# Performance work log

Measured on AMD Instinct MI355X. Metric: run time of the kernel, lower is better.

Reference implementation:

```python
import jax, jax.numpy as jnp
import numpy as np

K_PERIODS = 4
PMAX = 64
MIN_PERIOD = 8


def setup_inputs() -> dict:
    key = jax.random.key(0)
    x = jax.random.normal(key, (32, 512, 64), dtype=jnp.float32)  # [B, T, N]
    return {"x": x}


def reference(x):
    """Dense, fixed-shape equivalent of PeriodicityTransform.forward (mask=None).

    Instead of a Python list of variable-shape PeriodGroup tiles, returns a
    padded tensor values[bn, k, c, p] where for each (sequence bn, freq rank k)
    with period P and cycles C, values[bn, k, :C, :P] equals the torch tile
    seqs[bn, T-C*P : T].reshape(C, P); entries outside (C, P) are zero.
    Also returns the integer periods and cycles per (bn, k).
    """
    B, T, N = x.shape
    BN = B * N
    seqs = jnp.transpose(x, (0, 2, 1)).reshape(BN, T)  # [BN, T]

    # top-k nonzero FFT frequencies (DC bin zeroed out)
    spec = jnp.fft.rfft(seqs, axis=-1)
    mag2 = spec.real ** 2 + spec.imag ** 2
    mag2 = mag2.at[..., 0].set(0.0)
    _, kidx = jax.lax.top_k(mag2, K_PERIODS)  # [BN, K]
    kidx = jnp.maximum(kidx, 1)

    # periods = clamp(T // f, min=MIN_PERIOD, max=PMAX); cycles = T // period
    periods = jnp.clip(T // kidx, MIN_PERIOD, PMAX)  # [BN, K]
    cycles = T // periods                              # [BN, K]

    cmax = T // MIN_PERIOD  # static upper bound on cycles
    i = jnp.arange(cmax)[:, None]   # cycle index  [Cmax, 1]
    j = jnp.arange(PMAX)[None, :]   # phase index  [1, Pmax]

    start = T - cycles * periods                                   # [BN, K]
    idx = start[..., None, None] + i * periods[..., None, None] + j  # [BN,K,Cmax,Pmax]
    idx = jnp.clip(idx, 0, T - 1)
    valid = (i < cycles[..., None, None]) & (j < periods[..., None, None])

    gathered = jnp.take_along_axis(
        seqs[:, None, :], idx.reshape(BN, K_PERIODS, -1), axis=-1
    ).reshape(BN, K_PERIODS, cmax, PMAX)
    values = jnp.where(valid, gathered, jnp.float32(0.0))
    return values, periods, cycles
```

## Files before the change

### kernel.cpp

```cpp
#include <hip/hip_runtime.h>
#include <math.h>

#define TT 512
#define KP 4

typedef unsigned long long u64;

__global__ __launch_bounds__(256) void periodicity_kernel(const float* __restrict__ x,
                                                          float* __restrict__ out) {
    const int bn   = blockIdx.x;
    const int tid  = threadIdx.x;
    const int lane = tid & 63;
    const int wid  = tid >> 6;
    const int b = bn >> 6;
    const int n = bn & 63;

    __shared__ float  row[TT];
    __shared__ float2 buf[TT];
    __shared__ float2 tw[TT];
    __shared__ u64    keys[256];
    __shared__ int    fin8[8];
    __shared__ double candV8[8];

    float sv, cv_;
    sincosf((float)(2.0 * M_PI / 512.0) * (float)tid, &sv, &cv_);
    tw[tid]       = make_float2(cv_, -sv);
    tw[tid + 256] = make_float2(-cv_, sv);

    const float* xb = x + (size_t)b * (TT * 64) + n;
    {
        float v0 = xb[(size_t)tid * 64];
        float v1 = xb[(size_t)(tid + 256) * 64];
        row[tid] = v0;  row[tid + 256] = v1;
        float sum = v0 + v1, dif = v0 - v1;
        buf[tid]       = make_float2(sum, 0.f);
        buf[tid + 256] = make_float2(dif * cv_, -dif * sv);
    }
    __syncthreads();

    #pragma unroll
    for (int stg = 0; stg < 4; ++stg) {
        if (tid < 128) {
            const int Q  = 64 >> (2 * stg);
            const int B4 = Q << 2;
            const int h  = tid >> 6;
            const int j  = tid & 63;
            const int g  = j >> (6 - 2 * stg);
            const int i  = j & (Q - 1);
            const int base = (h << 8) + g * B4 + i;
            float2 x0 = buf[base], x1 = buf[base + Q];
            float2 x2 = buf[base + 2 * Q], x3 = buf[base + 3 * Q];
            float2 A  = make_float2(x0.x + x2.x, x0.y + x2.y);
            float2 Bm = make_float2(x0.x - x2.x, x0.y - x2.y);
            float2 Cc = make_float2(x1.x + x3.x, x1.y + x3.y);
            float2 D  = make_float2(x1.x - x3.x, x1.y - x3.y);
            float2 y0 = make_float2(A.x + Cc.x, A.y + Cc.y);
            float2 y2 = make_float2(A.x - Cc.x, A.y - Cc.y);
            float2 y1 = make_float2(Bm.x + D.y, Bm.y - D.x);
            float2 y3 = make_float2(Bm.x - D.y, Bm.y + D.x);
            const int m = i << (1 + 2 * stg);
            float2 t1 = tw[m], t2 = tw[2 * m], t3 = tw[3 * m];
            buf[base]         = y0;
            buf[base + Q]     = make_float2(y1.x * t1.x - y1.y * t1.y, y1.x * t1.y + y1.y * t1.x);
            buf[base + 2 * Q] = make_float2(y2.x * t2.x - y2.y * t2.y, y2.x * t2.y + y2.y * t2.x);
            buf[base + 3 * Q] = make_float2(y3.x * t3.x - y3.y * t3.y, y3.x * t3.y + y3.y * t3.x);
        }
        __syncthreads();
    }

    #pragma unroll
    for (int hh = 0; hh < 2; ++hh) {
        int pos = tid + hh * 256;
        int p = pos & 255;
        int kprime = ((p & 3) << 6) | (((p >> 2) & 3) << 4) | (((p >> 4) & 3) << 2) | ((p >> 6) & 3);
        int f = 2 * kprime + hh;
        if (f >= 1 && f <= 256) {
            float2 v = buf[pos];
            float mag = v.x * v.x + v.y * v.y;
            keys[f - 1] = ((u64)__float_as_uint(mag) << 32) | (u64)(255 - (f - 1));
        }
    }
    __syncthreads();

    if (wid == 0) {
        u64 k0 = keys[lane * 4 + 0];
        u64 k1 = keys[lane * 4 + 1];
        u64 k2 = keys[lane * 4 + 2];
        u64 k3 = keys[lane * 4 + 3];
        #define CSWAP(a, b) { if (a < b) { u64 _t = a; a = b; b = _t; } }
        CSWAP(k0, k1) CSWAP(k2, k3) CSWAP(k0, k2) CSWAP(k1, k3) CSWAP(k1, k2)
        #undef CSWAP
        #pragma unroll
        for (int r = 0; r < 8; ++r) {
            u64 w = k0;
            #pragma unroll
            for (int off = 32; off >= 1; off >>= 1) {
                u64 o = __shfl_xor(w, off);
                if (o > w) w = o;
            }
            if (k0 == w) { k0 = k1; k1 = k2; k2 = k3; k3 = 0; }
            if (lane == 0) fin8[r] = 256 - (int)(w & 0xff);
        }
    }
    __syncthreads();

    {
        const int cid = tid >> 5;
        const int sub = tid & 31;
        const int fc  = fin8[cid];
        const int t0  = sub * 16;
        const double W = 6.2831853071795864769 / 512.0;
        double zr, zi, wr, wi;
        sincos(W * (double)((fc * t0) & 511), &zi, &zr);
        sincos(W * (double)fc, &wi, &wr);
        double ar = 0.0, ai = 0.0;
        const float4* r4 = (const float4*)row;
        #pragma unroll
        for (int v4i = 0; v4i < 4; ++v4i) {
            float4 xv = r4[sub * 4 + v4i];
            #define STEP(comp)                                   \
                { double xd = (double)xv.comp;                   \
                  ar = fma(xd, zr, ar); ai = fma(xd, zi, ai);    \
                  double tq = zr * wr - zi * wi;                 \
                  zi = fma(zr, wi, zi * wr); zr = tq; }
            STEP(x) STEP(y) STEP(z) STEP(w)
            #undef STEP
        }
        #pragma unroll
        for (int off = 16; off >= 1; off >>= 1) {
            ar += __shfl_xor(ar, off);
            ai += __shfl_xor(ai, off);
        }
        if (sub == 0) candV8[cid] = ar * ar + ai * ai;
    }
    __syncthreads();

    int per[KP], cyc[KP], st[KP];
    {
        unsigned chosen = 0;
        #pragma unroll
        for (int k = 0; k < KP; ++k) {
            double bv = -1.0; int bbin = 0x7fffffff; int bj = 0;
            #pragma unroll
            for (int j = 0; j < 8; ++j) {
                if (chosen & (1u << j)) continue;
                double vj = candV8[j];
                int    bjn = fin8[j];
                if (vj > bv || (vj == bv && bjn < bbin)) { bv = vj; bbin = bjn; bj = j; }
            }
            chosen |= (1u << bj);
            int p = TT / bbin;
            p = p < 8 ? 8 : (p > 64 ? 64 : p);
            per[k] = p;
            cyc[k] = TT / p;
            st[k]  = TT - cyc[k] * p;
        }
    }

    const size_t VOFF = (size_t)2048 * KP * 64 * 64;
    if (tid == 0) {
        #pragma unroll
        for (int k = 0; k < KP; ++k) {
            out[VOFF + (size_t)bn * KP + k]        = (float)per[k];
            out[VOFF + 8192 + (size_t)bn * KP + k] = (float)cyc[k];
        }
    }

    float* outv = out + (size_t)bn * (KP * 64 * 64);
    const int c_local = tid >> 4;
    const int p0 = (tid & 15) << 2;
    #pragma unroll
    for (int it = 0; it < 16; ++it) {
        const int k = it >> 2;
        const int c = ((it & 3) << 4) + c_local;
        float4 v = make_float4(0.f, 0.f, 0.f, 0.f);
        const int P = per[k], C = cyc[k], S0 = st[k];
        if (c < C) {
            const int base = S0 + c * P;
            if (p0 + 3 < P) {
                v.x = row[base + p0];
                v.y = row[base + p0 + 1];
                v.z = row[base + p0 + 2];
                v.w = row[base + p0 + 3];
            } else {
                v.x = (p0 + 0 < P) ? row[base + p0]     : 0.f;
                v.y = (p0 + 1 < P) ? row[base + p0 + 1] : 0.f;
                v.z = (p0 + 2 < P) ? row[base + p0 + 2] : 0.f;
                v.w = (p0 + 3 < P) ? row[base + p0 + 3] : 0.f;
            }
        }
        *(float4*)(outv + (size_t)it * 1024 + (size_t)tid * 4) = v;
    }
}

extern "C" void kernel_launch(void* const* d_in, const int* in_sizes, int n_in,
                              void* d_out, int out_size, void* d_ws, size_t ws_size,
                              hipStream_t stream) {
    const float* x = (const float*)d_in[0];
    float* out = (float*)d_out;
    hipLaunchKernelGGL(periodicity_kernel, dim3(2048), dim3(256), 0, stream, x, out);
}
```

Baseline: 33.73 us.

## Process four sequences per block with float4 loads and two-row concurrent FFT

```diff
diff --git a/kernel.cpp b/kernel.cpp
--- a/kernel.cpp
+++ b/kernel.cpp
@@ -8,188 +8,207 @@
 
 __global__ __launch_bounds__(256) void periodicity_kernel(const float* __restrict__ x,
                                                           float* __restrict__ out) {
-    const int bn   = blockIdx.x;
+    const int blk  = blockIdx.x;
     const int tid  = threadIdx.x;
     const int lane = tid & 63;
     const int wid  = tid >> 6;
-    const int b = bn >> 6;
-    const int n = bn & 63;
-
-    __shared__ float  row[TT];
-    __shared__ float2 buf[TT];
+    const int b  = blk >> 4;
+    const int n0 = (blk & 15) << 2;
+
     __shared__ float2 tw[TT];
-    __shared__ u64    keys[256];
-    __shared__ int    fin8[8];
-    __shared__ double candV8[8];
-
-    float sv, cv_;
-    sincosf((float)(2.0 * M_PI / 512.0) * (float)tid, &sv, &cv_);
-    tw[tid]       = make_float2(cv_, -sv);
-    tw[tid + 256] = make_float2(-cv_, sv);
-
-    const float* xb = x + (size_t)b * (TT * 64) + n;
-    {
-        float v0 = xb[(size_t)tid * 64];
-        float v1 = xb[(size_t)(tid + 256) * 64];
-        row[tid] = v0;  row[tid + 256] = v1;
-        float sum = v0 + v1, dif = v0 - v1;
-        buf[tid]       = make_float2(sum, 0.f);
-        buf[tid + 256] = make_float2(dif * cv_, -dif * sv);
-    }
-    __syncthreads();
+    __shared__ float  rowl[2][TT];
+    __shared__ float2 buf[2][TT];
+    __shared__ u64    keys[2][256];
+    __shared__ int    fin8[2][8];
+    __shared__ double candV8[2][8];
+
+    float sv, cv;
+    sincosf((float)(2.0 * M_PI / 512.0) * (float)tid, &sv, &cv);
+    tw[tid]       = make_float2(cv, -sv);
+    tw[tid + 256] = make_float2(-cv, sv);
+
+    const float* xb = x + (size_t)b * (TT * 64) + n0;
+    float4 ldA = *(const float4*)(xb + (size_t)tid * 64);
+    float4 ldB = *(const float4*)(xb + (size_t)(tid + 256) * 64);
+
+    const size_t VOFF = (size_t)2048 * KP * 64 * 64;
 
     #pragma unroll
-    for (int stg = 0; stg < 4; ++stg) {
-        if (tid < 128) {
-            const int Q  = 64 >> (2 * stg);
-            const int B4 = Q << 2;
-            const int h  = tid >> 6;
-            const int j  = tid & 63;
-            const int g  = j >> (6 - 2 * stg);
-            const int i  = j & (Q - 1);
-            const int base = (h << 8) + g * B4 + i;
-            float2 x0 = buf[base], x1 = buf[base + Q];
-            float2 x2 = buf[base + 2 * Q], x3 = buf[base + 3 * Q];
-            float2 A  = make_float2(x0.x + x2.x, x0.y + x2.y);
-            float2 Bm = make_float2(x0.x - x2.x, x0.y - x2.y);
-            float2 Cc = make_float2(x1.x + x3.x, x1.y + x3.y);
-            float2 D  = make_float2(x1.x - x3.x, x1.y - x3.y);
-            float2 y0 = make_float2(A.x + Cc.x, A.y + Cc.y);
-            float2 y2 = make_float2(A.x - Cc.x, A.y - Cc.y);
-            float2 y1 = make_float2(Bm.x + D.y, Bm.y - D.x);
-            float2 y3 = make_float2(Bm.x - D.y, Bm.y + D.x);
-            const int m = i << (1 + 2 * stg);
-            float2 t1 = tw[m], t2 = tw[2 * m], t3 = tw[3 * m];
-            buf[base]         = y0;
-            buf[base + Q]     = make_float2(y1.x * t1.x - y1.y * t1.y, y1.x * t1.y + y1.y * t1.x);
-            buf[base + 2 * Q] = make_float2(y2.x * t2.x - y2.y * t2.y, y2.x * t2.y + y2.y * t2.x);
-            buf[base + 3 * Q] = make_float2(y3.x * t3.x - y3.y * t3.y, y3.x * t3.y + y3.y * t3.x);
-        }
-        __syncthreads();
-    }
-
-    #pragma unroll
-    for (int hh = 0; hh < 2; ++hh) {
-        int pos = tid + hh * 256;
-        int p = pos & 255;
-        int kprime = ((p & 3) << 6) | (((p >> 2) & 3) << 4) | (((p >> 4) & 3) << 2) | ((p >> 6) & 3);
-        int f = 2 * kprime + hh;
-        if (f >= 1 && f <= 256) {
-            float2 v = buf[pos];
-            float mag = v.x * v.x + v.y * v.y;
-            keys[f - 1] = ((u64)__float_as_uint(mag) << 32) | (u64)(255 - (f - 1));
-        }
-    }
-    __syncthreads();
-
-    if (wid == 0) {
-        u64 k0 = keys[lane * 4 + 0];
-        u64 k1 = keys[lane * 4 + 1];
-        u64 k2 = keys[lane * 4 + 2];
-        u64 k3 = keys[lane * 4 + 3];
-        #define CSWAP(a, b) { if (a < b) { u64 _t = a; a = b; b = _t; } }
-        CSWAP(k0, k1) CSWAP(k2, k3) CSWAP(k0, k2) CSWAP(k1, k3) CSWAP(k1, k2)
-        #undef CSWAP
+    for (int ss = 0; ss < 2; ++ss) {
+        __syncthreads();
+
         #pragma unroll
-        for (int r = 0; r < 8; ++r) {
-            u64 w = k0;
-            #pragma unroll
-            for (int off = 32; off >= 1; off >>= 1) {
-                u64 o = __shfl_xor(w, off);
-                if (o > w) w = o;
-            }
-            if (k0 == w) { k0 = k1; k1 = k2; k2 = k3; k3 = 0; }
-            if (lane == 0) fin8[r] = 256 - (int)(w & 0xff);
-        }
-    }
-    __syncthreads();
-
-    {
-        const int cid = tid >> 5;
-        const int sub = tid & 31;
-        const int fc  = fin8[cid];
-        const int t0  = sub * 16;
-        const double W = 6.2831853071795864769 / 512.0;
-        double zr, zi, wr, wi;
-        sincos(W * (double)((fc * t0) & 511), &zi, &zr);
-        sincos(W * (double)fc, &wi, &wr);
-        double ar = 0.0, ai = 0.0;
-        const float4* r4 = (const float4*)row;
+        for (int rr = 0; rr < 2; ++rr) {
+            const int rg = ss * 2 + rr;
+            float v0 = ((const float*)&ldA)[rg];
+            float v1 = ((const float*)&ldB)[rg];
+            rowl[rr][tid] = v0;  rowl[rr][tid + 256] = v1;
+            float sum = v0 + v1, dif = v0 - v1;
+            buf[rr][tid]       = make_float2(sum, 0.f);
+            buf[rr][tid + 256] = make_float2(dif * cv, -dif * sv);
+        }
+        __syncthreads();
+
+        {
+            const int frr = tid >> 7;
+            const int fh  = (tid >> 6) & 1;
+            const int fj  = tid & 63;
+            float2* bb = &buf[frr][fh << 8];
+            #pragma unroll
+            for (int stg = 0; stg < 4; ++stg) {
+                const int Q  = 64 >> (2 * stg);
+                const int B4 = Q << 2;
+                const int g  = fj >> (6 - 2 * stg);
+                const int i  = fj & (Q - 1);
+                const int base = g * B4 + i;
+                float2 x0 = bb[base],         x1 = bb[base + Q];
+                float2 x2 = bb[base + 2 * Q], x3 = bb[base + 3 * Q];
+                float2 A  = make_float2(x0.x + x2.x, x0.y + x2.y);
+                float2 Bm = make_float2(x0.x - x2.x, x0.y - x2.y);
+                float2 Cc = make_float2(x1.x + x3.x, x1.y + x3.y);
+                float2 D  = make_float2(x1.x - x3.x, x1.y - x3.y);
+                float2 y0 = make_float2(A.x + Cc.x, A.y + Cc.y);
+                float2 y2 = make_float2(A.x - Cc.x, A.y - Cc.y);
+                float2 y1 = make_float2(Bm.x + D.y, Bm.y - D.x);
+                float2 y3 = make_float2(Bm.x - D.y, Bm.y + D.x);
+                const int m = i << (1 + 2 * stg);
+                float2 t1 = tw[m], t2 = tw[2 * m], t3 = tw[3 * m];
+                bb[base]         = y0;
+                bb[base + Q]     = make_float2(y1.x * t1.x - y1.y * t1.y, y1.x * t1.y + y1.y * t1.x);
+                bb[base + 2 * Q] = make_float2(y2.x * t2.x - y2.y * t2.y, y2.x * t2.y + y2.y * t2.x);
+                bb[base + 3 * Q] = make_float2(y3.x * t3.x - y3.y * t3.y, y3.x * t3.y + y3.y * t3.x);
+                __syncthreads();
+            }
+        }
+
+        {
+            const int p  = tid;
+            const int kp = ((p & 3) << 6) | (((p >> 2) & 3) << 4) | (((p >> 4) & 3) << 2) | ((p >> 6) & 3);
+            #pragma unroll
+            for (int q = 0; q < 4; ++q) {
+                const int rr = q >> 1, hh = q & 1;
+                const int f = 2 * kp + hh;
+                if (f >= 1 && f <= 256) {
+                    float2 v = buf[rr][hh * 256 + p];
+                    float mag = v.x * v.x + v.y * v.y;
+                    keys[rr][f - 1] = ((u64)__float_as_uint(mag) << 32) | (u64)(255 - (f - 1));
+                }
+            }
+        }
+        __syncthreads();
+
+        if (wid < 2) {
+            const int rr = wid;
+            u64 k0 = keys[rr][lane * 4 + 0];
+            u64 k1 = keys[rr][lane * 4 + 1];
+            u64 k2 = keys[rr][lane * 4 + 2];
+            u64 k3 = keys[rr][lane * 4 + 3];
+            #define CSWAP(a, b) { if (a < b) { u64 _t = a; a = b; b = _t; } }
+            CSWAP(k0, k1) CSWAP(k2, k3) CSWAP(k0, k2) CSWAP(k1, k3) CSWAP(k1, k2)
+            #undef CSWAP
+            #pragma unroll
+            for (int r = 0; r < 8; ++r) {
+                u64 w = k0;
+                #pragma unroll
+                for (int off = 32; off >= 1; off >>= 1) {
+                    u64 o = __shfl_xor(w, off);
+                    if (o > w) w = o;
+                }
+                if (k0 == w) { k0 = k1; k1 = k2; k2 = k3; k3 = 0; }
+                if (lane == 0) fin8[rr][r] = 256 - (int)(w & 0xff);
+            }
+        }
+        __syncthreads();
+
+        {
+            const int cidg = tid >> 4;
+            const int rr   = cidg >> 3;
+            const int cand = cidg & 7;
+            const int sub  = tid & 15;
+            const int fc = fin8[rr][cand];
+            const int t0 = sub * 32;
+            const double W = 6.2831853071795864769 / 512.0;
+            double zr, zi, wr, wi;
+            sincos(W * (double)((fc * t0) & 511), &zi, &zr);
+            sincos(W * (double)fc, &wi, &wr);
+            double ar = 0.0, ai = 0.0;
+            const float4* r4 = (const float4*)rowl[rr];
+            #pragma unroll
+            for (int v4i = 0; v4i < 8; ++v4i) {
+                float4 xv = r4[sub * 8 + v4i];
+                #define STEP(comp)                                   \
+                    { double xd = (double)xv.comp;                   \
+                      ar = fma(xd, zr, ar); ai = fma(xd, zi, ai);    \
+                      double tq = zr * wr - zi * wi;                 \
+                      zi = fma(zr, wi, zi * wr); zr = tq; }
+                STEP(x) STEP(y) STEP(z) STEP(w)
+                #undef STEP
+            }
+            #pragma unroll
+            for (int off = 8; off >= 1; off >>= 1) {
+                ar += __shfl_xor(ar, off);
+                ai += __shfl_xor(ai, off);
+            }
+            if (sub == 0) candV8[rr][cand] = ar * ar + ai * ai;
+        }
+        __syncthreads();
+
         #pragma unroll
-        for (int v4i = 0; v4i < 4; ++v4i) {
-            float4 xv = r4[sub * 4 + v4i];
-            #define STEP(comp)                                   \
-                { double xd = (double)xv.comp;                   \
-                  ar = fma(xd, zr, ar); ai = fma(xd, zi, ai);    \
-                  double tq = zr * wr - zi * wi;                 \
-                  zi = fma(zr, wi, zi * wr); zr = tq; }
-            STEP(x) STEP(y) STEP(z) STEP(w)
-            #undef STEP
-        }
-        #pragma unroll
-        for (int off = 16; off >= 1; off >>= 1) {
-            ar += __shfl_xor(ar, off);
-            ai += __shfl_xor(ai, off);
-        }
-        if (sub == 0) candV8[cid] = ar * ar + ai * ai;
-    }
-    __syncthreads();
-
-    int per[KP], cyc[KP], st[KP];
-    {
-        unsigned chosen = 0;
-        #pragma unroll
-        for (int k = 0; k < KP; ++k) {
-            double bv = -1.0; int bbin = 0x7fffffff; int bj = 0;
-            #pragma unroll
-            for (int j = 0; j < 8; ++j) {
-                if (chosen & (1u << j)) continue;
-                double vj = candV8[j];
-                int    bjn = fin8[j];
-                if (vj > bv || (vj == bv && bjn < bbin)) { bv = vj; bbin = bjn; bj = j; }
-            }
-            chosen |= (1u << bj);
-            int p = TT / bbin;
-            p = p < 8 ? 8 : (p > 64 ? 64 : p);
-            per[k] = p;
-            cyc[k] = TT / p;
-            st[k]  = TT - cyc[k] * p;
-        }
-    }
-
-    const size_t VOFF = (size_t)2048 * KP * 64 * 64;
-    if (tid == 0) {
-        #pragma unroll
-        for (int k = 0; k < KP; ++k) {
-            out[VOFF + (size_t)bn * KP + k]        = (float)per[k];
-            out[VOFF + 8192 + (size_t)bn * KP + k] = (float)cyc[k];
-        }
-    }
-
-    float* outv = out + (size_t)bn * (KP * 64 * 64);
-    const int c_local = tid >> 4;
-    const int p0 = (tid & 15) << 2;
-    #pragma unroll
-    for (int it = 0; it < 16; ++it) {
-        const int k = it >> 2;
-        const int c = ((it & 3) << 4) + c_local;
-        float4 v = make_float4(0.f, 0.f, 0.f, 0.f);
-        const int P = per[k], C = cyc[k], S0 = st[k];
-        if (c < C) {
-            const int base = S0 + c * P;
-            if (p0 + 3 < P) {
-                v.x = row[base + p0];
-                v.y = row[base + p0 + 1];
-                v.z = row[base + p0 + 2];
-                v.w = row[base + p0 + 3];
-            } else {
-                v.x = (p0 + 0 < P) ? row[base + p0]     : 0.f;
-                v.y = (p0 + 1 < P) ? row[base + p0 + 1] : 0.f;
-                v.z = (p0 + 2 < P) ? row[base + p0 + 2] : 0.f;
-                v.w = (p0 + 3 < P) ? row[base + p0 + 3] : 0.f;
-            }
-        }
-        *(float4*)(outv + (size_t)it * 1024 + (size_t)tid * 4) = v;
+        for (int rr = 0; rr < 2; ++rr) {
+            const int rg = ss * 2 + rr;
+            const int bn = b * 64 + n0 + rg;
+            int per[KP], cycv[KP], st[KP];
+            unsigned chosen = 0;
+            #pragma unroll
+            for (int k = 0; k < KP; ++k) {
+                double bv = -1.0; int bbin = 0x7fffffff; int bj = 0;
+                #pragma unroll
+                for (int j = 0; j < 8; ++j) {
+                    if (chosen & (1u << j)) continue;
+                    double vj = candV8[rr][j];
+                    int    bjn = fin8[rr][j];
+                    if (vj > bv || (vj == bv && bjn < bbin)) { bv = vj; bbin = bjn; bj = j; }
+                }
+                chosen |= (1u << bj);
+                int p = TT / bbin;
+                p = p < 8 ? 8 : (p > 64 ? 64 : p);
+                per[k]  = p;
+                cycv[k] = TT / p;
+                st[k]   = TT - cycv[k] * p;
+            }
+            if (tid == 0) {
+                #pragma unroll
+                for (int k = 0; k < KP; ++k) {
+                    out[VOFF + (size_t)bn * KP + k]        = (float)per[k];
+                    out[VOFF + 8192 + (size_t)bn * KP + k] = (float)cycv[k];
+                }
+            }
+            float* outv = out + (size_t)bn * (KP * 64 * 64);
+            const int c_local = tid >> 4;
+            const int p0 = (tid & 15) << 2;
+            #pragma unroll
+            for (int it = 0; it < 16; ++it) {
+                const int k = it >> 2;
+                const int c = ((it & 3) << 4) + c_local;
+                float4 v = make_float4(0.f, 0.f, 0.f, 0.f);
+                const int P = per[k], C = cycv[k], S0 = st[k];
+                if (c < C) {
+                    const int base = S0 + c * P;
+                    if (p0 + 3 < P) {
+                        v.x = rowl[rr][base + p0];
+                        v.y = rowl[rr][base + p0 + 1];
+                        v.z = rowl[rr][base + p0 + 2];
+                        v.w = rowl[rr][base + p0 + 3];
+                    } else {
+                        v.x = (p0 + 0 < P) ? rowl[rr][base + p0]     : 0.f;
+                        v.y = (p0 + 1 < P) ? rowl[rr][base + p0 + 1] : 0.f;
+                        v.z = (p0 + 2 < P) ? rowl[rr][base + p0 + 2] : 0.f;
+                        v.w = (p0 + 3 < P) ? rowl[rr][base + p0 + 3] : 0.f;
+                    }
+                }
+                *(float4*)(outv + (size_t)it * 1024 + (size_t)tid * 4) = v;
+            }
+        }
     }
 }
 
@@ -198,5 +217,5 @@
                               hipStream_t stream) {
     const float* x = (const float*)d_in[0];
     float* out = (float*)d_out;
-    hipLaunchKernelGGL(periodicity_kernel, dim3(2048), dim3(256), 0, stream, x, out);
+    hipLaunchKernelGGL(periodicity_kernel, dim3(512), dim3(256), 0, stream, x, out);
 }
```

Result: slower. 43.27 us (+28.3%).

## Process four sequences per block with float4 loads and overlapped output stores

Applied to the files above, without the earlier changes.

```diff
diff --git a/kernel.cpp b/kernel.cpp
--- a/kernel.cpp
+++ b/kernel.cpp
@@ -6,191 +6,219 @@
 
 typedef unsigned long long u64;
 
-__global__ __launch_bounds__(256) void periodicity_kernel(const float* __restrict__ x,
+__global__ __launch_bounds__(512) void periodicity_kernel(const float* __restrict__ x,
                                                           float* __restrict__ out) {
-    const int bn   = blockIdx.x;
+    const int blk  = blockIdx.x;
     const int tid  = threadIdx.x;
     const int lane = tid & 63;
     const int wid  = tid >> 6;
-    const int b = bn >> 6;
-    const int n = bn & 63;
-
-    __shared__ float  row[TT];
+    const int b  = blk >> 4;
+    const int n0 = (blk & 15) << 2;
+
+    __shared__ float2 tw[TT];
+    __shared__ __align__(16) float rowl[2][TT];
     __shared__ float2 buf[TT];
-    __shared__ float2 tw[TT];
     __shared__ u64    keys[256];
     __shared__ int    fin8[8];
     __shared__ double candV8[8];
-
-    float sv, cv_;
-    sincosf((float)(2.0 * M_PI / 512.0) * (float)tid, &sv, &cv_);
-    tw[tid]       = make_float2(cv_, -sv);
-    tw[tid + 256] = make_float2(-cv_, sv);
-
-    const float* xb = x + (size_t)b * (TT * 64) + n;
+    __shared__ int    pstore[2][12];
+
     {
-        float v0 = xb[(size_t)tid * 64];
-        float v1 = xb[(size_t)(tid + 256) * 64];
-        row[tid] = v0;  row[tid + 256] = v1;
-        float sum = v0 + v1, dif = v0 - v1;
-        buf[tid]       = make_float2(sum, 0.f);
-        buf[tid + 256] = make_float2(dif * cv_, -dif * sv);
+        float s, c;
+        sincosf((float)(2.0 * M_PI / 512.0) * (float)tid, &s, &c);
+        tw[tid] = make_float2(c, -s);
     }
-    __syncthreads();
+
+    const float* xb = x + (size_t)b * (TT * 64) + n0;
+    float4 ld = *(const float4*)(xb + (size_t)tid * 64);
+
+    const size_t VOFF = (size_t)2048 * KP * 64 * 64;
+
+    auto store_row = [&](int rowIdx, int pvb) {
+        const int bnp = b * 64 + n0 + rowIdx;
+        float* outv = out + (size_t)bnp * (KP * 64 * 64);
+        #pragma unroll
+        for (int it = 0; it < 8; ++it) {
+            const int flat4 = it * 512 + tid;
+            const int k   = flat4 >> 10;
+            const int rem = flat4 & 1023;
+            const int c   = rem >> 4;
+            const int p0  = (rem & 15) << 2;
+            const int P = pstore[pvb][k], C = pstore[pvb][4 + k], S0 = pstore[pvb][8 + k];
+            float4 v = make_float4(0.f, 0.f, 0.f, 0.f);
+            if (c < C) {
+                const int base = S0 + c * P;
+                if (p0 + 3 < P) {
+                    v.x = rowl[pvb][base + p0];
+                    v.y = rowl[pvb][base + p0 + 1];
+                    v.z = rowl[pvb][base + p0 + 2];
+                    v.w = rowl[pvb][base + p0 + 3];
+                } else {
+                    if (p0     < P) v.x = rowl[pvb][base + p0];
+                    if (p0 + 1 < P) v.y = rowl[pvb][base + p0 + 1];
+                    if (p0 + 2 < P) v.z = rowl[pvb][base + p0 + 2];
+                    if (p0 + 3 < P) v.w = rowl[pvb][base + p0 + 3];
+                }
+            }
+            *(float4*)(outv + (size_t)flat4 * 4) = v;
+        }
+    };
 
     #pragma unroll
-    for (int stg = 0; stg < 4; ++stg) {
-        if (tid < 128) {
-            const int Q  = 64 >> (2 * stg);
-            const int B4 = Q << 2;
-            const int h  = tid >> 6;
-            const int j  = tid & 63;
-            const int g  = j >> (6 - 2 * stg);
-            const int i  = j & (Q - 1);
-            const int base = (h << 8) + g * B4 + i;
-            float2 x0 = buf[base], x1 = buf[base + Q];
-            float2 x2 = buf[base + 2 * Q], x3 = buf[base + 3 * Q];
-            float2 A  = make_float2(x0.x + x2.x, x0.y + x2.y);
-            float2 Bm = make_float2(x0.x - x2.x, x0.y - x2.y);
-            float2 Cc = make_float2(x1.x + x3.x, x1.y + x3.y);
-            float2 D  = make_float2(x1.x - x3.x, x1.y - x3.y);
-            float2 y0 = make_float2(A.x + Cc.x, A.y + Cc.y);
-            float2 y2 = make_float2(A.x - Cc.x, A.y - Cc.y);
-            float2 y1 = make_float2(Bm.x + D.y, Bm.y - D.x);
-            float2 y3 = make_float2(Bm.x - D.y, Bm.y + D.x);
-            const int m = i << (1 + 2 * stg);
-            float2 t1 = tw[m], t2 = tw[2 * m], t3 = tw[3 * m];
-            buf[base]         = y0;
-            buf[base + Q]     = make_float2(y1.x * t1.x - y1.y * t1.y, y1.x * t1.y + y1.y * t1.x);
-            buf[base + 2 * Q] = make_float2(y2.x * t2.x - y2.y * t2.y, y2.x * t2.y + y2.y * t2.x);
-            buf[base + 3 * Q] = make_float2(y3.x * t3.x - y3.y * t3.y, y3.x * t3.y + y3.y * t3.x);
+    for (int ss = 0; ss < 4; ++ss) {
+        const int cur = ss & 1, pv = cur ^ 1;
+
+        if (ss > 0) store_row(ss - 1, pv);
+
+        {
+            float rv = (ss == 0) ? ld.x : (ss == 1) ? ld.y : (ss == 2) ? ld.z : ld.w;
+            rowl[cur][tid] = rv;
+        }
+        __syncthreads();
+
+        if (tid < 256) {
+            buf[tid] = make_float2(rowl[cur][tid] + rowl[cur][tid + 256], 0.f);
+        } else {
+            const int j = tid - 256;
+            float dif = rowl[cur][j] - rowl[cur][j + 256];
+            float2 t = tw[j];
+            buf[tid] = make_float2(dif * t.x, dif * t.y);
+        }
+        __syncthreads();
+
+        #pragma unroll
+        for (int stg = 0; stg < 4; ++stg) {
+            if (tid < 128) {
+                const int Q  = 64 >> (2 * stg);
+                const int B4 = Q << 2;
+                const int h  = tid >> 6;
+                const int fj = tid & 63;
+                const int g  = fj >> (6 - 2 * stg);
+                const int i  = fj & (Q - 1);
+                float2* bb = &buf[h << 8];
+                const int base = g * B4 + i;
+                float2 x0 = bb[base],         x1 = bb[base + Q];
+                float2 x2 = bb[base + 2 * Q], x3 = bb[base + 3 * Q];
+                float2 A  = make_float2(x0.x + x2.x, x0.y + x2.y);
+                float2 Bm = make_float2(x0.x - x2.x, x0.y - x2.y);
+                float2 Cc = make_float2(x1.x + x3.x, x1.y + x3.y);
+                float2 D  = make_float2(x1.x - x3.x, x1.y - x3.y);
+                float2 y0 = make_float2(A.x + Cc.x, A.y + Cc.y);
+                float2 y2 = make_float2(A.x - Cc.x, A.y - Cc.y);
+                float2 y1 = make_float2(Bm.x + D.y, Bm.y - D.x);
+                float2 y3 = make_float2(Bm.x - D.y, Bm.y + D.x);
+                const int m = i << (1 + 2 * stg);
+                float2 t1 = tw[m], t2 = tw[2 * m], t3 = tw[3 * m];
+                bb[base]         = y0;
+                bb[base + Q]     = make_float2(y1.x * t1.x - y1.y * t1.y, y1.x * t1.y + y1.y * t1.x);
+                bb[base + 2 * Q] = make_float2(y2.x * t2.x - y2.y * t2.y, y2.x * t2.y + y2.y * t2.x);
+                bb[base + 3 * Q] = make_float2(y3.x * t3.x - y3.y * t3.y, y3.x * t3.y + y3.y * t3.x);
+            }
+            __syncthreads();
+        }
+
+        {
+            const int p  = tid & 255;
+            const int hh = tid >> 8;
+            const int kp = ((p & 3) << 6) | (((p >> 2) & 3) << 4) | (((p >> 4) & 3) << 2) | ((p >> 6) & 3);
+            const int f = 2 * kp + hh;
+            if (f >= 1 && f <= 256) {
+                float2 v = buf[tid];
+                float mag = v.x * v.x + v.y * v.y;
+                keys[f - 1] = ((u64)__float_as_uint(mag) << 32) | (u64)(255 - (f - 1));
+            }
+        }
+        __syncthreads();
+
+        if (wid == 0) {
+            u64 k0 = keys[lane * 4 + 0];
+            u64 k1 = keys[lane * 4 + 1];
+            u64 k2 = keys[lane * 4 + 2];
+            u64 k3 = keys[lane * 4 + 3];
+            #define CSWAP(a, b) { if (a < b) { u64 _t = a; a = b; b = _t; } }
+            CSWAP(k0, k1) CSWAP(k2, k3) CSWAP(k0, k2) CSWAP(k1, k3) CSWAP(k1, k2)
+            #undef CSWAP
+            #pragma unroll
+            for (int r = 0; r < 8; ++r) {
+                u64 w = k0;
+                #pragma unroll
+                for (int off = 32; off >= 1; off >>= 1) {
+                    u64 o = __shfl_xor(w, off);
+                    if (o > w) w = o;
+                }
+                if (k0 == w) { k0 = k1; k1 = k2; k2 = k3; k3 = 0; }
+                if (lane == 0) fin8[r] = 256 - (int)(w & 0xff);
+            }
+        }
+        __syncthreads();
+
+        if (tid < 256) {
+            const int cid = tid >> 5;
+            const int sub = tid & 31;
+            const int fc  = fin8[cid];
+            const int t0  = sub * 16;
+            const double W = 6.2831853071795864769 / 512.0;
+            double zr, zi, wr, wi;
+            sincos(W * (double)((fc * t0) & 511), &zi, &zr);
+            sincos(W * (double)fc, &wi, &wr);
+            double ar = 0.0, ai = 0.0;
+            const float4* r4 = (const float4*)rowl[cur];
+            #pragma unroll
+            for (int v4i = 0; v4i < 4; ++v4i) {
+                float4 xv = r4[sub * 4 + v4i];
+                #define STEP(comp)                                   \
+                    { double xd = (double)xv.comp;                   \
+                      ar = fma(xd, zr, ar); ai = fma(xd, zi, ai);    \
+                      double tq = zr * wr - zi * wi;                 \
+                      zi = fma(zr, wi, zi * wr); zr = tq; }
+                STEP(x) STEP(y) STEP(z) STEP(w)
+                #undef STEP
+            }
+            #pragma unroll
+            for (int off = 16; off >= 1; off >>= 1) {
+                ar += __shfl_xor(ar, off);
+                ai += __shfl_xor(ai, off);
+            }
+            if (sub == 0) candV8[cid] = ar * ar + ai * ai;
+        }
+        __syncthreads();
+
+        if (wid == 0) {
+            int per[KP], cycv[KP], stv[KP];
+            unsigned chosen = 0;
+            #pragma unroll
+            for (int k = 0; k < KP; ++k) {
+                double bv = -1.0; int bbin = 0x7fffffff; int bj = 0;
+                #pragma unroll
+                for (int j = 0; j < 8; ++j) {
+                    if (chosen & (1u << j)) continue;
+                    double vj = candV8[j];
+                    int    bjn = fin8[j];
+                    if (vj > bv || (vj == bv && bjn < bbin)) { bv = vj; bbin = bjn; bj = j; }
+                }
+                chosen |= (1u << bj);
+                int p = TT / bbin;
+                p = p < 8 ? 8 : (p > 64 ? 64 : p);
+                per[k]  = p;
+                cycv[k] = TT / p;
+                stv[k]  = TT - cycv[k] * p;
+            }
+            if (lane == 0) {
+                const int bn = b * 64 + n0 + ss;
+                #pragma unroll
+                for (int k = 0; k < KP; ++k) {
+                    pstore[cur][k]     = per[k];
+                    pstore[cur][4 + k] = cycv[k];
+                    pstore[cur][8 + k] = stv[k];
+                    out[VOFF + (size_t)bn * KP + k]        = (float)per[k];
+                    out[VOFF + 8192 + (size_t)bn * KP + k] = (float)cycv[k];
+                }
+            }
         }
         __syncthreads();
     }
 
-    #pragma unroll
-    for (int hh = 0; hh < 2; ++hh) {
-        int pos = tid + hh * 256;
-        int p = pos & 255;
-        int kprime = ((p & 3) << 6) | (((p >> 2) & 3) << 4) | (((p >> 4) & 3) << 2) | ((p >> 6) & 3);
-        int f = 2 * kprime + hh;
-        if (f >= 1 && f <= 256) {
-            float2 v = buf[pos];
-            float mag = v.x * v.x + v.y * v.y;
-            keys[f - 1] = ((u64)__float_as_uint(mag) << 32) | (u64)(255 - (f - 1));
-        }
-    }
-    __syncthreads();
-
-    if (wid == 0) {
-        u64 k0 = keys[lane * 4 + 0];
-        u64 k1 = keys[lane * 4 + 1];
-        u64 k2 = keys[lane * 4 + 2];
-        u64 k3 = keys[lane * 4 + 3];
-        #define CSWAP(a, b) { if (a < b) { u64 _t = a; a = b; b = _t; } }
-        CSWAP(k0, k1) CSWAP(k2, k3) CSWAP(k0, k2) CSWAP(k1, k3) CSWAP(k1, k2)
-        #undef CSWAP
-        #pragma unroll
-        for (int r = 0; r < 8; ++r) {
-            u64 w = k0;
-            #pragma unroll
-            for (int off = 32; off >= 1; off >>= 1) {
-                u64 o = __shfl_xor(w, off);
-                if (o > w) w = o;
-            }
-            if (k0 == w) { k0 = k1; k1 = k2; k2 = k3; k3 = 0; }
-            if (lane == 0) fin8[r] = 256 - (int)(w & 0xff);
-        }
-    }
-    __syncthreads();
-
-    {
-        const int cid = tid >> 5;
-        const int sub = tid & 31;
-        const int fc  = fin8[cid];
-        const int t0  = sub * 16;
-        const double W = 6.2831853071795864769 / 512.0;
-        double zr, zi, wr, wi;
-        sincos(W * (double)((fc * t0) & 511), &zi, &zr);
-        sincos(W * (double)fc, &wi, &wr);
-        double ar = 0.0, ai = 0.0;
-        const float4* r4 = (const float4*)row;
-        #pragma unroll
-        for (int v4i = 0; v4i < 4; ++v4i) {
-            float4 xv = r4[sub * 4 + v4i];
-            #define STEP(comp)                                   \
-                { double xd = (double)xv.comp;                   \
-                  ar = fma(xd, zr, ar); ai = fma(xd, zi, ai);    \
-                  double tq = zr * wr - zi * wi;                 \
-                  zi = fma(zr, wi, zi * wr); zr = tq; }
-            STEP(x) STEP(y) STEP(z) STEP(w)
-            #undef STEP
-        }
-        #pragma unroll
-        for (int off = 16; off >= 1; off >>= 1) {
-            ar += __shfl_xor(ar, off);
-            ai += __shfl_xor(ai, off);
-        }
-        if (sub == 0) candV8[cid] = ar * ar + ai * ai;
-    }
-    __syncthreads();
-
-    int per[KP], cyc[KP], st[KP];
-    {
-        unsigned chosen = 0;
-        #pragma unroll
-        for (int k = 0; k < KP; ++k) {
-            double bv = -1.0; int bbin = 0x7fffffff; int bj = 0;
-            #pragma unroll
-            for (int j = 0; j < 8; ++j) {
-                if (chosen & (1u << j)) continue;
-                double vj = candV8[j];
-                int    bjn = fin8[j];
-                if (vj > bv || (vj == bv && bjn < bbin)) { bv = vj; bbin = bjn; bj = j; }
-            }
-            chosen |= (1u << bj);
-            int p = TT / bbin;
-            p = p < 8 ? 8 : (p > 64 ? 64 : p);
-            per[k] = p;
-            cyc[k] = TT / p;
-            st[k]  = TT - cyc[k] * p;
-        }
-    }
-
-    const size_t VOFF = (size_t)2048 * KP * 64 * 64;
-    if (tid == 0) {
-        #pragma unroll
-        for (int k = 0; k < KP; ++k) {
-            out[VOFF + (size_t)bn * KP + k]        = (float)per[k];
-            out[VOFF + 8192 + (size_t)bn * KP + k] = (float)cyc[k];
-        }
-    }
-
-    float* outv = out + (size_t)bn * (KP * 64 * 64);
-    const int c_local = tid >> 4;
-    const int p0 = (tid & 15) << 2;
-    #pragma unroll
-    for (int it = 0; it < 16; ++it) {
-        const int k = it >> 2;
-        const int c = ((it & 3) << 4) + c_local;
-        float4 v = make_float4(0.f, 0.f, 0.f, 0.f);
-        const int P = per[k], C = cyc[k], S0 = st[k];
-        if (c < C) {
-            const int base = S0 + c * P;
-            if (p0 + 3 < P) {
-                v.x = row[base + p0];
-                v.y = row[base + p0 + 1];
-                v.z = row[base + p0 + 2];
-                v.w = row[base + p0 + 3];
-            } else {
-                v.x = (p0 + 0 < P) ? row[base + p0]     : 0.f;
-                v.y = (p0 + 1 < P) ? row[base + p0 + 1] : 0.f;
-                v.z = (p0 + 2 < P) ? row[base + p0 + 2] : 0.f;
-                v.w = (p0 + 3 < P) ? row[base + p0 + 3] : 0.f;
-            }
-        }
-        *(float4*)(outv + (size_t)it * 1024 + (size_t)tid * 4) = v;
-    }
+    store_row(3, 1);
 }
 
 extern "C" void kernel_launch(void* const* d_in, const int* in_sizes, int n_in,
@@ -198,5 +226,5 @@
                               hipStream_t stream) {
     const float* x = (const float*)d_in[0];
     float* out = (float*)d_out;
-    hipLaunchKernelGGL(periodicity_kernel, dim3(2048), dim3(256), 0, stream, x, out);
+    hipLaunchKernelGGL(periodicity_kernel, dim3(512), dim3(512), 0, stream, x, out);
 }
```

Measured after the change: 47.86 us. 1.42x slower.

## Skip fp64 DFT refinement when top magnitudes are well separated; hoist zero fill

Applied to the files above, without the earlier changes.

```diff
diff --git a/kernel.cpp b/kernel.cpp
--- a/kernel.cpp
+++ b/kernel.cpp
@@ -5,6 +5,8 @@
 #define KP 4
 
 typedef unsigned long long u64;
+
+#define SYNCL() asm volatile("s_waitcnt lgkmcnt(0)\n\ts_barrier" ::: "memory")
 
 __global__ __launch_bounds__(256) void periodicity_kernel(const float* __restrict__ x,
                                                           float* __restrict__ out) {
@@ -15,17 +17,24 @@
     const int b = bn >> 6;
     const int n = bn & 63;
 
-    __shared__ float  row[TT];
+    __shared__ float2 tw[TT];
+    __shared__ __align__(16) float row[TT];
     __shared__ float2 buf[TT];
-    __shared__ float2 tw[TT];
     __shared__ u64    keys[256];
     __shared__ int    fin8[8];
+    __shared__ float  candMagF[8];
     __shared__ double candV8[8];
-
-    float sv, cv_;
-    sincosf((float)(2.0 * M_PI / 512.0) * (float)tid, &sv, &cv_);
-    tw[tid]       = make_float2(cv_, -sv);
-    tw[tid + 256] = make_float2(-cv_, sv);
+    __shared__ unsigned char w4tab[64];
+
+    float sv, cv;
+    sincosf((float)(2.0 * M_PI / 512.0) * (float)tid, &sv, &cv);
+    tw[tid]       = make_float2(cv, -sv);
+    tw[tid + 256] = make_float2(-cv, sv);
+    if (tid < 64) {
+        int W = 512 / (tid + 1);
+        W = W < 8 ? 8 : (W > 64 ? 64 : W);
+        w4tab[tid] = (unsigned char)((W + 3) >> 2);
+    }
 
     const float* xb = x + (size_t)b * (TT * 64) + n;
     {
@@ -34,9 +43,25 @@
         row[tid] = v0;  row[tid + 256] = v1;
         float sum = v0 + v1, dif = v0 - v1;
         buf[tid]       = make_float2(sum, 0.f);
-        buf[tid + 256] = make_float2(dif * cv_, -dif * sv);
-    }
-    __syncthreads();
+        buf[tid + 256] = make_float2(dif * cv, -dif * sv);
+    }
+    SYNCL();
+
+    float* outv = out + (size_t)bn * (KP * 64 * 64);
+    {
+        const int j  = tid & 15;
+        const int cb = tid >> 4;
+        #pragma unroll
+        for (int iter = 0; iter < 4; ++iter) {
+            const int c = 8 + iter * 16 + cb;
+            if (c < 64 && j >= (int)w4tab[c]) {
+                const float4 z = make_float4(0.f, 0.f, 0.f, 0.f);
+                #pragma unroll
+                for (int k = 0; k < KP; ++k)
+                    *(float4*)(outv + k * 4096 + c * 64 + j * 4) = z;
+            }
+        }
+    }
 
     #pragma unroll
     for (int stg = 0; stg < 4; ++stg) {
@@ -44,12 +69,13 @@
             const int Q  = 64 >> (2 * stg);
             const int B4 = Q << 2;
             const int h  = tid >> 6;
-            const int j  = tid & 63;
-            const int g  = j >> (6 - 2 * stg);
-            const int i  = j & (Q - 1);
-            const int base = (h << 8) + g * B4 + i;
-            float2 x0 = buf[base], x1 = buf[base + Q];
-            float2 x2 = buf[base + 2 * Q], x3 = buf[base + 3 * Q];
+            const int fj = tid & 63;
+            const int g  = fj >> (6 - 2 * stg);
+            const int i  = fj & (Q - 1);
+            float2* bb = &buf[h << 8];
+            const int base = g * B4 + i;
+            float2 x0 = bb[base],         x1 = bb[base + Q];
+            float2 x2 = bb[base + 2 * Q], x3 = bb[base + 3 * Q];
             float2 A  = make_float2(x0.x + x2.x, x0.y + x2.y);
             float2 Bm = make_float2(x0.x - x2.x, x0.y - x2.y);
             float2 Cc = make_float2(x1.x + x3.x, x1.y + x3.y);
@@ -60,27 +86,26 @@
             float2 y3 = make_float2(Bm.x - D.y, Bm.y + D.x);
             const int m = i << (1 + 2 * stg);
             float2 t1 = tw[m], t2 = tw[2 * m], t3 = tw[3 * m];
-            buf[base]         = y0;
-            buf[base + Q]     = make_float2(y1.x * t1.x - y1.y * t1.y, y1.x * t1.y + y1.y * t1.x);
-            buf[base + 2 * Q] = make_float2(y2.x * t2.x - y2.y * t2.y, y2.x * t2.y + y2.y * t2.x);
-            buf[base + 3 * Q] = make_float2(y3.x * t3.x - y3.y * t3.y, y3.x * t3.y + y3.y * t3.x);
-        }
-        __syncthreads();
+            bb[base]         = y0;
+            bb[base + Q]     = make_float2(y1.x * t1.x - y1.y * t1.y, y1.x * t1.y + y1.y * t1.x);
+            bb[base + 2 * Q] = make_float2(y2.x * t2.x - y2.y * t2.y, y2.x * t2.y + y2.y * t2.x);
+            bb[base + 3 * Q] = make_float2(y3.x * t3.x - y3.y * t3.y, y3.x * t3.y + y3.y * t3.x);
+        }
+        SYNCL();
     }
 
     #pragma unroll
     for (int hh = 0; hh < 2; ++hh) {
-        int pos = tid + hh * 256;
-        int p = pos & 255;
-        int kprime = ((p & 3) << 6) | (((p >> 2) & 3) << 4) | (((p >> 4) & 3) << 2) | ((p >> 6) & 3);
-        int f = 2 * kprime + hh;
+        const int p = tid;
+        const int kp = ((p & 3) << 6) | (((p >> 2) & 3) << 4) | (((p >> 4) & 3) << 2) | ((p >> 6) & 3);
+        const int f = 2 * kp + hh;
         if (f >= 1 && f <= 256) {
-            float2 v = buf[pos];
+            float2 v = buf[hh * 256 + p];
             float mag = v.x * v.x + v.y * v.y;
             keys[f - 1] = ((u64)__float_as_uint(mag) << 32) | (u64)(255 - (f - 1));
         }
     }
-    __syncthreads();
+    SYNCL();
 
     if (wid == 0) {
         u64 k0 = keys[lane * 4 + 0];
@@ -99,61 +124,77 @@
                 if (o > w) w = o;
             }
             if (k0 == w) { k0 = k1; k1 = k2; k2 = k3; k3 = 0; }
-            if (lane == 0) fin8[r] = 256 - (int)(w & 0xff);
-        }
-    }
-    __syncthreads();
-
-    {
-        const int cid = tid >> 5;
-        const int sub = tid & 31;
-        const int fc  = fin8[cid];
-        const int t0  = sub * 16;
-        const double W = 6.2831853071795864769 / 512.0;
-        double zr, zi, wr, wi;
-        sincos(W * (double)((fc * t0) & 511), &zi, &zr);
-        sincos(W * (double)fc, &wi, &wr);
-        double ar = 0.0, ai = 0.0;
-        const float4* r4 = (const float4*)row;
-        #pragma unroll
-        for (int v4i = 0; v4i < 4; ++v4i) {
-            float4 xv = r4[sub * 4 + v4i];
-            #define STEP(comp)                                   \
-                { double xd = (double)xv.comp;                   \
-                  ar = fma(xd, zr, ar); ai = fma(xd, zi, ai);    \
-                  double tq = zr * wr - zi * wi;                 \
-                  zi = fma(zr, wi, zi * wr); zr = tq; }
-            STEP(x) STEP(y) STEP(z) STEP(w)
-            #undef STEP
-        }
-        #pragma unroll
-        for (int off = 16; off >= 1; off >>= 1) {
-            ar += __shfl_xor(ar, off);
-            ai += __shfl_xor(ai, off);
-        }
-        if (sub == 0) candV8[cid] = ar * ar + ai * ai;
-    }
-    __syncthreads();
-
-    int per[KP], cyc[KP], st[KP];
-    {
-        unsigned chosen = 0;
+            if (lane == 0) {
+                fin8[r] = 256 - (int)(w & 0xff);
+                candMagF[r] = __uint_as_float((unsigned)(w >> 32));
+            }
+        }
+    }
+    SYNCL();
+
+    int per[KP], cycv[KP], stv[KP];
+    {
+        const float m0 = candMagF[0], m1 = candMagF[1], m2 = candMagF[2],
+                    m3 = candMagF[3], m4 = candMagF[4];
+        const bool needRefine = ((m0 - m1) <= 1e-4f * m0) || ((m1 - m2) <= 1e-4f * m1) ||
+                                ((m2 - m3) <= 1e-4f * m2) || ((m3 - m4) <= 1e-4f * m3);
+        int bins[KP];
+        if (!needRefine) {
+            #pragma unroll
+            for (int k = 0; k < KP; ++k) bins[k] = fin8[k];
+        } else {
+            {
+                const int cid = tid >> 5;
+                const int sub = tid & 31;
+                const int fc  = fin8[cid];
+                const int t0  = sub * 16;
+                const double W = 6.2831853071795864769 / 512.0;
+                double zr, zi, wr, wi;
+                sincos(W * (double)((fc * t0) & 511), &zi, &zr);
+                sincos(W * (double)fc, &wi, &wr);
+                double ar = 0.0, ai = 0.0;
+                const float4* r4 = (const float4*)row;
+                #pragma unroll
+                for (int v4i = 0; v4i < 4; ++v4i) {
+                    float4 xv = r4[sub * 4 + v4i];
+                    #define STEP(comp)                                   \
+                        { double xd = (double)xv.comp;                   \
+                          ar = fma(xd, zr, ar); ai = fma(xd, zi, ai);    \
+                          double tq = zr * wr - zi * wi;                 \
+                          zi = fma(zr, wi, zi * wr); zr = tq; }
+                    STEP(x) STEP(y) STEP(z) STEP(w)
+                    #undef STEP
+                }
+                #pragma unroll
+                for (int off = 16; off >= 1; off >>= 1) {
+                    ar += __shfl_xor(ar, off);
+                    ai += __shfl_xor(ai, off);
+                }
+                if (sub == 0) candV8[cid] = ar * ar + ai * ai;
+            }
+            SYNCL();
+            unsigned chosen = 0;
+            #pragma unroll
+            for (int k = 0; k < KP; ++k) {
+                double bv = -1.0; int bbin = 0x7fffffff; int bj = 0;
+                #pragma unroll
+                for (int j = 0; j < 8; ++j) {
+                    if (chosen & (1u << j)) continue;
+                    double vj = candV8[j];
+                    int    bjn = fin8[j];
+                    if (vj > bv || (vj == bv && bjn < bbin)) { bv = vj; bbin = bjn; bj = j; }
+                }
+                chosen |= (1u << bj);
+                bins[k] = bbin;
+            }
+        }
         #pragma unroll
         for (int k = 0; k < KP; ++k) {
-            double bv = -1.0; int bbin = 0x7fffffff; int bj = 0;
-            #pragma unroll
-            for (int j = 0; j < 8; ++j) {
-                if (chosen & (1u << j)) continue;
-                double vj = candV8[j];
-                int    bjn = fin8[j];
-                if (vj > bv || (vj == bv && bjn < bbin)) { bv = vj; bbin = bjn; bj = j; }
-            }
-            chosen |= (1u << bj);
-            int p = TT / bbin;
+            int p = TT / bins[k];
             p = p < 8 ? 8 : (p > 64 ? 64 : p);
-            per[k] = p;
-            cyc[k] = TT / p;
-            st[k]  = TT - cyc[k] * p;
+            per[k]  = p;
+            cycv[k] = TT / p;
+            stv[k]  = TT - cycv[k] * p;
         }
     }
 
@@ -162,34 +203,35 @@
         #pragma unroll
         for (int k = 0; k < KP; ++k) {
             out[VOFF + (size_t)bn * KP + k]        = (float)per[k];
-            out[VOFF + 8192 + (size_t)bn * KP + k] = (float)cyc[k];
-        }
-    }
-
-    float* outv = out + (size_t)bn * (KP * 64 * 64);
-    const int c_local = tid >> 4;
-    const int p0 = (tid & 15) << 2;
-    #pragma unroll
-    for (int it = 0; it < 16; ++it) {
-        const int k = it >> 2;
-        const int c = ((it & 3) << 4) + c_local;
-        float4 v = make_float4(0.f, 0.f, 0.f, 0.f);
-        const int P = per[k], C = cyc[k], S0 = st[k];
-        if (c < C) {
+            out[VOFF + 8192 + (size_t)bn * KP + k] = (float)cycv[k];
+        }
+    }
+
+    {
+        const int c  = tid >> 2;
+        const int j0 = tid & 3;
+        const int W4c = (int)w4tab[c];
+        #pragma unroll
+        for (int k = 0; k < KP; ++k) {
+            const int P = per[k], C = cycv[k], S0 = stv[k];
+            const int inC  = (c < C) ? 1 : 0;
             const int base = S0 + c * P;
-            if (p0 + 3 < P) {
-                v.x = row[base + p0];
-                v.y = row[base + p0 + 1];
-                v.z = row[base + p0 + 2];
-                v.w = row[base + p0 + 3];
-            } else {
-                v.x = (p0 + 0 < P) ? row[base + p0]     : 0.f;
-                v.y = (p0 + 1 < P) ? row[base + p0 + 1] : 0.f;
-                v.z = (p0 + 2 < P) ? row[base + p0 + 2] : 0.f;
-                v.w = (p0 + 3 < P) ? row[base + p0 + 3] : 0.f;
-            }
-        }
-        *(float4*)(outv + (size_t)it * 1024 + (size_t)tid * 4) = v;
+            #pragma unroll
+            for (int m = 0; m < 4; ++m) {
+                const int j = j0 + (m << 2);
+                if (j < W4c) {
+                    const int p0 = j << 2;
+                    float4 v = make_float4(0.f, 0.f, 0.f, 0.f);
+                    if (inC) {
+                        if (p0     < P) v.x = row[base + p0];
+                        if (p0 + 1 < P) v.y = row[base + p0 + 1];
+                        if (p0 + 2 < P) v.z = row[base + p0 + 2];
+                        if (p0 + 3 < P) v.w = row[base + p0 + 3];
+                    }
+                    *(float4*)(outv + k * 4096 + c * 64 + p0) = v;
+                }
+            }
+        }
     }
 }
 
```

Result: slower. 35.75 us (+6.0%).
